# Kernel optimization log

Measured on AMD Instinct MI355X. Metric: run time of the kernel, lower is better.

Reference implementation:

```python
import jax, jax.numpy as jnp
import numpy as np
import math

N, D = 4096, 1024


def setup_inputs() -> dict:
    key = jax.random.key(0)
    ks = jax.random.split(key, 8)
    vecs = jax.random.normal(ks[0], (N, D), dtype=jnp.float32)
    mass = jax.random.uniform(ks[1], (N,), dtype=jnp.float32)            # semantic mass in [0,1)
    hops = jax.random.uniform(ks[2], (N,), dtype=jnp.float32) * 5.0      # hop distances in [0,5)
    alive = jax.random.randint(ks[3], (N,), 0, 10) > 0
    is_photon = jax.random.randint(ks[4], (N,), 0, 10) == 0
    W_res_w = jax.random.normal(ks[5], (D, D), dtype=jnp.float32) / np.sqrt(D)
    W_res_b = jnp.zeros((D,), dtype=jnp.float32)
    w_conf_i = jax.random.normal(ks[6], (D,), dtype=jnp.float32) / np.sqrt(2 * D)
    w_conf_j = jax.random.normal(ks[7], (D,), dtype=jnp.float32) / np.sqrt(2 * D)
    b_conf = jnp.zeros((), dtype=jnp.float32)
    log_c = jnp.asarray(math.log(50.0), dtype=jnp.float32)  # 'relationship' domain
    log_G = jnp.zeros((), dtype=jnp.float32)
    return dict(vecs=vecs, mass=mass, hops=hops, alive=alive, is_photon=is_photon,
                W_res_w=W_res_w, W_res_b=W_res_b, w_conf_i=w_conf_i, w_conf_j=w_conf_j,
                b_conf=b_conf, log_c=log_c, log_G=log_G)


def reference(vecs, mass, hops, alive, is_photon, W_res_w, W_res_b,
              w_conf_i, w_conf_j, b_conf, log_c, log_G):
    n = vecs.shape[0]
    c = jnp.maximum(jnp.exp(log_c), 1e-6)
    G = jnp.exp(log_G)

    # Per-row quantities (phi() reads hops/photon from entity i).
    d_light = hops / c                                                   # [N]
    lam = jnp.where(is_photon, 1.0, jnp.exp(-d_light))                   # redshift, [N]
    r2 = jnp.maximum(d_light, 0.1) ** 2                                  # r_safe^2, [N]
    causal_decay = jnp.where(d_light <= 1.0, 1.0, jnp.exp(-d_light + 1.0))  # [N]

    # Causal mask: j must be strictly in the past (j < i).
    idx = jnp.arange(n)
    past = (idx[None, :] < idx[:, None]).astype(vecs.dtype)              # [N,N]
    C = past * causal_decay[:, None]

    # Gravity: G * m_i * m_j / r_i^2
    grav = G * (mass / r2)[:, None] * mass[None, :]                      # [N,N]

    # Resonance: cosine similarity of W_res projections (torch eps=1e-8 norm clamp).
    v = vecs @ W_res_w.T + W_res_b                                       # [N,D]
    vn = v / jnp.maximum(jnp.linalg.norm(v, axis=-1, keepdims=True), 1e-8)
    R = vn @ vn.T                                                        # [N,N]
    zero_norm = jnp.linalg.norm(vecs, axis=-1) < 1e-8                    # [N]
    R = jnp.where(zero_norm[:, None] | zero_norm[None, :], 0.0, R)

    # Conflict gate: sigmoid(W_conflict @ concat(v_i, v_j) + b) = sigmoid(s_i + s_j + b).
    s_i = vecs @ w_conf_i                                                # [N]
    s_j = vecs @ w_conf_j                                                # [N]
    conflict = jax.nn.sigmoid(s_i[:, None] + s_j[None, :] + b_conf)      # [N,N]

    phi_attract = lam[:, None] * grav * C * (0.5 + 0.5 * R)
    phi_repulse = -lam[:, None] * conflict * mass[:, None] * mass[None, :]
    phi = jnp.where(conflict > 0.8, phi_repulse, phi_attract)

    # Black holes and the diagonal produce zero field.
    gate = alive[:, None] & alive[None, :]
    phi = jnp.where(gate & (idx[:, None] != idx[None, :]), phi, 0.0)
    return phi
```

## Files before the change

### kernel.cpp

```cpp
#include <hip/hip_runtime.h>
#include <hip/hip_bf16.h>
#include <math.h>

#define NROW 4096
#define DIM  1024

typedef short v8s __attribute__((ext_vector_type(8)));
typedef float v4f __attribute__((ext_vector_type(4)));

#define GLD16(src, dst) __builtin_amdgcn_global_load_lds( \
    (const __attribute__((address_space(1))) void*)(src), \
    (__attribute__((address_space(3))) void*)(dst), 16, 0, 0)

__device__ __forceinline__ ushort f2bf(float f) {
    __hip_bfloat16 h = __float2bfloat16(f);
    union { __hip_bfloat16 h; ushort u; } x; x.h = h; return x.u;
}
__device__ __forceinline__ ushort4 cvt4(float4 a) {
    ushort4 r; r.x = f2bf(a.x); r.y = f2bf(a.y); r.z = f2bf(a.z); r.w = f2bf(a.w);
    return r;
}

__global__ __launch_bounds__(256) void k_stats(
    const float* __restrict__ vecs, const float* __restrict__ mass,
    const float* __restrict__ hops, const int* __restrict__ alive,
    const int* __restrict__ is_photon, const float* __restrict__ wci,
    const float* __restrict__ wcj, const float* __restrict__ logc,
    const float* __restrict__ logG, const float* __restrict__ bconf,
    const float* __restrict__ W,
    double* __restrict__ s_i, double* __restrict__ s_j,
    float* __restrict__ rowAtt, float* __restrict__ rowRep,
    float* __restrict__ massF, int* __restrict__ flags,
    float* __restrict__ rownorm)
{
    const int t = threadIdx.x;
    const int wid = t >> 6, lane = t & 63;

    if (blockIdx.x >= NROW / 4) {
        const int row = (blockIdx.x - NROW / 4) * 4 + wid;
        const float* wr = W + (size_t)row * DIM;
        ushort4 uc[4];
        #pragma unroll
        for (int q = 0; q < 4; ++q)
            uc[q] = cvt4(*(const float4*)&wr[lane * 4 + q * 256]);
        __syncthreads();
        ushort* wb = (ushort*)W + (size_t)row * 2048 + 1024;
        #pragma unroll
        for (int q = 0; q < 4; ++q)
            *(ushort4*)&wb[lane * 4 + q * 256] = uc[q];
        return;
    }

    const int row = blockIdx.x * 4 + wid;
    const float* vr = vecs + (size_t)row * DIM;
    double di = 0.0, dj = 0.0, ss = 0.0;
    ushort4 uc[4];
    #pragma unroll
    for (int q = 0; q < 4; ++q) {
        int base = lane * 4 + q * 256;
        float4 pv = *(const float4*)&vr[base];
        float4 pi = *(const float4*)&wci[base];
        float4 pj = *(const float4*)&wcj[base];
        di += (double)pv.x * pi.x + (double)pv.y * pi.y + (double)pv.z * pi.z + (double)pv.w * pi.w;
        dj += (double)pv.x * pj.x + (double)pv.y * pj.y + (double)pv.z * pj.z + (double)pv.w * pj.w;
        ss += (double)pv.x * pv.x + (double)pv.y * pv.y + (double)pv.z * pv.z + (double)pv.w * pv.w;
        uc[q] = cvt4(pv);
    }
    __syncthreads();
    ushort* vb = (ushort*)vecs + (size_t)row * 2048 + 1024;
    #pragma unroll
    for (int q = 0; q < 4; ++q)
        *(ushort4*)&vb[lane * 4 + q * 256] = uc[q];
    #pragma unroll
    for (int off = 32; off > 0; off >>= 1) {
        di += __shfl_down(di, off);
        dj += __shfl_down(dj, off);
        ss += __shfl_down(ss, off);
    }
    if (lane == 0) {
        double c  = fmax(exp((double)logc[0]), 1e-6);
        double G  = exp((double)logG[0]);
        double dl = (double)hops[row] / c;
        double lam = (is_photon[row] != 0) ? 1.0 : exp(-dl);
        double rs  = fmax(dl, 0.1);
        double cd  = (dl <= 1.0) ? 1.0 : exp(-dl + 1.0);
        double m   = (double)mass[row];
        s_i[row] = di;
        s_j[row] = dj + (double)bconf[0];
        rowAtt[row] = (float)(lam * G * m / (rs * rs) * cd);
        rowRep[row] = (float)(-lam * m);
        massF[row]  = (float)m;
        flags[row]  = ((alive[row] != 0) ? 1 : 0) | ((sqrt(ss) < 1e-8) ? 2 : 0);
        rownorm[row] = 0.0f;
    }
}

__global__ __launch_bounds__(256) void k_proj(
    const float* __restrict__ A, const float* __restrict__ B,
    const float* __restrict__ bias, ushort* __restrict__ vout,
    float* __restrict__ rownorm)
{
    __shared__ ushort As[64 * 64], Bs[64 * 64];
    const int t = threadIdx.x;
    const int m0 = blockIdx.y * 64, n0 = blockIdx.x * 64;
    const int wid = t >> 6, lane = t & 63;
    const int wm = wid >> 1, wn = wid & 1;
    const int quad = lane >> 4, l16 = lane & 15;
    const ushort* Ab = (const ushort*)A;
    const ushort* Bb = (const ushort*)B;
    const int sr = t >> 3;
    const int sc = t & 7;
    v4f acc[2][2];
    #pragma unroll
    for (int i = 0; i < 2; i++)
        #pragma unroll
        for (int j = 0; j < 2; j++) acc[i][j] = (v4f){0.f, 0.f, 0.f, 0.f};

    for (int k0 = 0; k0 < DIM; k0 += 64) {
        #pragma unroll
        for (int p = 0; p < 2; ++p) {
            int r = p * 32 + sr;
            int ksw = ((sc ^ (r & 7)) * 8);
            GLD16(&Ab[(size_t)(m0 + r) * 2048 + 1024 + k0 + ksw], &As[p * 2048 + wid * 512]);
            GLD16(&Bb[(size_t)(n0 + r) * 2048 + 1024 + k0 + ksw], &Bs[p * 2048 + wid * 512]);
        }
        __syncthreads();
        #pragma unroll
        for (int ks = 0; ks < 2; ++ks) {
            v8s af[2], bfr[2];
            #pragma unroll
            for (int mi = 0; mi < 2; mi++) {
                int row = wm * 32 + mi * 16 + l16;
                af[mi] = *(const v8s*)&As[row * 64 + (((ks * 4 + quad) ^ (l16 & 7)) * 8)];
            }
            #pragma unroll
            for (int ni = 0; ni < 2; ni++) {
                int row = wn * 32 + ni * 16 + l16;
                bfr[ni] = *(const v8s*)&Bs[row * 64 + (((ks * 4 + quad) ^ (l16 & 7)) * 8)];
            }
            #pragma unroll
            for (int mi = 0; mi < 2; mi++)
                #pragma unroll
                for (int ni = 0; ni < 2; ni++)
                    acc[mi][ni] = __builtin_amdgcn_mfma_f32_16x16x32_bf16(af[mi], bfr[ni], acc[mi][ni], 0, 0, 0);
        }
        __syncthreads();
    }
    float bcol[2];
    #pragma unroll
    for (int ni = 0; ni < 2; ni++) bcol[ni] = bias[n0 + wn * 32 + ni * 16 + l16];
    #pragma unroll
    for (int mi = 0; mi < 2; mi++)
        #pragma unroll
        for (int r = 0; r < 4; r++) {
            int row = m0 + wm * 32 + mi * 16 + quad * 4 + r;
            float ss = 0.0f;
            #pragma unroll
            for (int ni = 0; ni < 2; ni++) {
                int col = n0 + wn * 32 + ni * 16 + l16;
                float vv = acc[mi][ni][r] + bcol[ni];
                vout[(size_t)row * DIM + col] = f2bf(vv);
                ss += vv * vv;
            }
            #pragma unroll
            for (int off = 8; off > 0; off >>= 1) ss += __shfl_down(ss, off);
            if (l16 == 0) atomicAdd(&rownorm[row], ss);
        }
}

__global__ __launch_bounds__(256) void k_phi(
    const ushort* __restrict__ vn,
    const double* __restrict__ s_i, const double* __restrict__ s_j,
    const float* __restrict__ rowAtt, const float* __restrict__ rowRep,
    const float* __restrict__ massF, const int* __restrict__ flags,
    const float* __restrict__ rownorm, float* __restrict__ out)
{
    __shared__ ushort As[128 * 64], Bs[128 * 64];
    const int t = threadIdx.x;
    const int id = blockIdx.x;
    int r = 0;
    while (id >= ((r + 1) * (r + 2)) >> 1) ++r;
    const int bi = r, bj = id - ((r * (r + 1)) >> 1);
    const int m0 = bi * 128, n0 = bj * 128;
    const int wid = t >> 6, lane = t & 63;
    const int wm = wid >> 1, wn = wid & 1;
    const int quad = lane >> 4, l16 = lane & 15;
    const double LN4 = 1.3862943611198906;

    if (id < 496) {
        int l = id, rl = 0;
        while (l >= 31 - rl) { l -= 31 - rl; ++rl; }
        const int lm0 = rl * 128, ln0 = (rl + 1 + l) * 128;
        float cmL[4]; double csjL[4]; int cfL[4]; int ccolL[4];
        #pragma unroll
        for (int ni = 0; ni < 4; ni++) {
            int col = ln0 + wn * 64 + ni * 16 + l16;
            ccolL[ni] = col; cmL[ni] = massF[col]; csjL[ni] = s_j[col]; cfL[ni] = flags[col];
        }
        #pragma unroll
        for (int mi = 0; mi < 4; mi++)
            #pragma unroll
            for (int rr = 0; rr < 4; rr++) {
                int row = lm0 + wm * 64 + mi * 16 + quad * 4 + rr;
                float  rR = rowRep[row];
                int    fi = flags[row];
                double si = s_i[row];
                size_t ob = (size_t)row * NROW;
                #pragma unroll
                for (int ni = 0; ni < 4; ni++) {
                    double x = si + csjL[ni];
                    bool   hit = (x > LN4) && ((fi & cfL[ni]) & 1);
                    float  conflict = 1.0f / (1.0f + expf(-(float)x));
                    out[ob + ccolL[ni]] = hit ? rR * conflict * cmL[ni] : 0.0f;
                }
            }
    }

    float  cm[4]; double csj[4]; int cf[4]; int ccol[4];
    #pragma unroll
    for (int ni = 0; ni < 4; ni++) {
        int col = n0 + wn * 64 + ni * 16 + l16;
        ccol[ni] = col; cm[ni] = massF[col]; csj[ni] = s_j[col]; cf[ni] = flags[col];
    }

    v4f acc[4][4];
    #pragma unroll
    for (int i = 0; i < 4; i++)
        #pragma unroll
        for (int j = 0; j < 4; j++) acc[i][j] = (v4f){0.f, 0.f, 0.f, 0.f};

    const int sr = t >> 3;
    const int sc = t & 7;
    for (int k0 = 0; k0 < DIM; k0 += 64) {
        #pragma unroll
        for (int p = 0; p < 4; ++p) {
            int rr = p * 32 + sr;
            int ksw = ((sc ^ (rr & 7)) * 8);
            GLD16(&vn[(size_t)(m0 + rr) * DIM + k0 + ksw], &As[p * 2048 + wid * 512]);
            GLD16(&vn[(size_t)(n0 + rr) * DIM + k0 + ksw], &Bs[p * 2048 + wid * 512]);
        }
        __syncthreads();
        #pragma unroll
        for (int ks = 0; ks < 2; ++ks) {
            v8s af[4], bfr[4];
            #pragma unroll
            for (int mi = 0; mi < 4; mi++) {
                int row = wm * 64 + mi * 16 + l16;
                af[mi] = *(const v8s*)&As[row * 64 + (((ks * 4 + quad) ^ (l16 & 7)) * 8)];
            }
            #pragma unroll
            for (int ni = 0; ni < 4; ni++) {
                int row = wn * 64 + ni * 16 + l16;
                bfr[ni] = *(const v8s*)&Bs[row * 64 + (((ks * 4 + quad) ^ (l16 & 7)) * 8)];
            }
            #pragma unroll
            for (int mi = 0; mi < 4; mi++)
                #pragma unroll
                for (int ni = 0; ni < 4; ni++)
                    acc[mi][ni] = __builtin_amdgcn_mfma_f32_16x16x32_bf16(af[mi], bfr[ni], acc[mi][ni], 0, 0, 0);
        }
        __syncthreads();
    }

    float cinv[4];
    #pragma unroll
    for (int ni = 0; ni < 4; ni++)
        cinv[ni] = 1.0f / fmaxf(sqrtf(rownorm[ccol[ni]]), 1e-8f);

    #pragma unroll
    for (int mi = 0; mi < 4; mi++)
        #pragma unroll
        for (int rr = 0; rr < 4; rr++) {
            int row = m0 + wm * 64 + mi * 16 + quad * 4 + rr;
            float  rA = rowAtt[row], rR = rowRep[row];
            float  riv = 1.0f / fmaxf(sqrtf(rownorm[row]), 1e-8f);
            int    fi = flags[row];
            double si = s_i[row];
            size_t ob = (size_t)row * NROW;
            #pragma unroll
            for (int ni = 0; ni < 4; ni++) {
                int col = ccol[ni];
                double x = si + csj[ni];
                float conflict = 1.0f / (1.0f + expf(-(float)x));
                bool  chigh = x > LN4;
                bool  gate  = ((fi & cf[ni]) & 1) && (row != col);
                float Rv  = ((fi | cf[ni]) & 2) ? 0.0f : acc[mi][ni][rr] * riv * cinv[ni];
                float att = (col < row) ? rA * cm[ni] * (0.5f + 0.5f * Rv) : 0.0f;
                float ph  = gate ? (chigh ? rR * conflict * cm[ni] : att) : 0.0f;
                out[ob + col] = ph;
            }
        }
}

extern "C" void kernel_launch(void* const* d_in, const int* in_sizes, int n_in,
                              void* d_out, int out_size, void* d_ws, size_t ws_size,
                              hipStream_t stream)
{
    const float* vecs      = (const float*)d_in[0];
    const float* mass      = (const float*)d_in[1];
    const float* hops      = (const float*)d_in[2];
    const int*   alive     = (const int*)d_in[3];
    const int*   is_photon = (const int*)d_in[4];
    const float* W         = (const float*)d_in[5];
    const float* Wb        = (const float*)d_in[6];
    const float* wci       = (const float*)d_in[7];
    const float* wcj       = (const float*)d_in[8];
    const float* bconf     = (const float*)d_in[9];
    const float* logc      = (const float*)d_in[10];
    const float* logG      = (const float*)d_in[11];

    char* ws = (char*)d_ws;
    double* s_i     = (double*)(ws);
    double* s_j     = (double*)(ws + 32768);
    float*  rowAtt  = (float*)(ws + 65536);
    float*  rowRep  = (float*)(ws + 81920);
    float*  massF   = (float*)(ws + 98304);
    int*    flagsA  = (int*)(ws + 114688);
    float*  rownorm = (float*)(ws + 131072);
    ushort* vn      = (ushort*)(ws + 147456);

    k_stats<<<dim3(NROW / 4 + DIM / 4), dim3(256), 0, stream>>>(
        vecs, mass, hops, alive, is_photon, wci, wcj, logc, logG, bconf, W,
        s_i, s_j, rowAtt, rowRep, massF, flagsA, rownorm);
    k_proj<<<dim3(DIM / 64, NROW / 64), dim3(256), 0, stream>>>(vecs, W, Wb, vn, rownorm);
    k_phi<<<dim3(528), dim3(256), 0, stream>>>(
        vn, s_i, s_j, rowAtt, rowRep, massF, flagsA, rownorm, (float*)d_out);
}
```

Baseline: 184.4 us.

## Shrink phi tiles to 64x64, fold mirror tile writes and precompute per-row/col factors

The phi kernel moves from 128x128 to 64x64 output tiles over the lower triangle (2080 blocks instead of 528). Each off-diagonal block now also writes the mirrored upper-triangle repulse-only tile, so a separate group of 496 blocks is no longer needed. Alive and zero-norm masks and the norm reciprocals are folded into precomputed per-row and per-column factors, and fast exp and rcp intrinsics replace the exact ones. The first K tile is prefetched before the loop and occupancy is raised with launch bounds, at the cost of less data reuse per block and more LDS barriers per unit of work.

```diff
diff --git a/kernel.cpp b/kernel.cpp
--- a/kernel.cpp
+++ b/kernel.cpp
@@ -168,126 +168,147 @@
         }
 }
 
-__global__ __launch_bounds__(256) void k_phi(
+__global__ __launch_bounds__(256, 5) void k_phi(
     const ushort* __restrict__ vn,
     const double* __restrict__ s_i, const double* __restrict__ s_j,
     const float* __restrict__ rowAtt, const float* __restrict__ rowRep,
     const float* __restrict__ massF, const int* __restrict__ flags,
     const float* __restrict__ rownorm, float* __restrict__ out)
 {
-    __shared__ ushort As[128 * 64], Bs[128 * 64];
+    __shared__ ushort As[64 * 64], Bs[64 * 64];
     const int t = threadIdx.x;
     const int id = blockIdx.x;
-    int r = 0;
-    while (id >= ((r + 1) * (r + 2)) >> 1) ++r;
+    int r = (int)((sqrtf(8.0f * (float)id + 1.0f) - 1.0f) * 0.5f);
+    while ((((r + 1) * (r + 2)) >> 1) <= id) ++r;
+    while (((r * (r + 1)) >> 1) > id) --r;
     const int bi = r, bj = id - ((r * (r + 1)) >> 1);
-    const int m0 = bi * 128, n0 = bj * 128;
+    const bool diag = (bi == bj);
+    const int m0 = bi * 64, n0 = bj * 64;
     const int wid = t >> 6, lane = t & 63;
     const int wm = wid >> 1, wn = wid & 1;
     const int quad = lane >> 4, l16 = lane & 15;
+    const int sr = t >> 3, sc = t & 7;
     const double LN4 = 1.3862943611198906;
 
-    if (id < 496) {
-        int l = id, rl = 0;
-        while (l >= 31 - rl) { l -= 31 - rl; ++rl; }
-        const int lm0 = rl * 128, ln0 = (rl + 1 + l) * 128;
-        float cmL[4]; double csjL[4]; int cfL[4]; int ccolL[4];
-        #pragma unroll
-        for (int ni = 0; ni < 4; ni++) {
-            int col = ln0 + wn * 64 + ni * 16 + l16;
-            ccolL[ni] = col; cmL[ni] = massF[col]; csjL[ni] = s_j[col]; cfL[ni] = flags[col];
-        }
-        #pragma unroll
-        for (int mi = 0; mi < 4; mi++)
+    #pragma unroll
+    for (int p = 0; p < 2; ++p) {
+        int rr = p * 32 + sr;
+        int ksw = (sc ^ (rr & 7)) * 8;
+        GLD16(&vn[(size_t)(m0 + rr) * DIM + ksw], &As[p * 2048 + wid * 512]);
+        GLD16(&vn[(size_t)(n0 + rr) * DIM + ksw], &Bs[p * 2048 + wid * 512]);
+    }
+
+    if (!diag) {
+        double csjL[2]; float cmL[2]; int colL[2];
+        #pragma unroll
+        for (int ni = 0; ni < 2; ni++) {
+            int col = m0 + wn * 32 + ni * 16 + l16;
+            colL[ni] = col;
+            csjL[ni] = s_j[col];
+            cmL[ni]  = (flags[col] & 1) ? massF[col] : 0.f;
+        }
+        #pragma unroll
+        for (int mi = 0; mi < 2; mi++)
             #pragma unroll
             for (int rr = 0; rr < 4; rr++) {
-                int row = lm0 + wm * 64 + mi * 16 + quad * 4 + rr;
-                float  rR = rowRep[row];
-                int    fi = flags[row];
+                int row = n0 + wm * 32 + mi * 16 + quad * 4 + rr;
                 double si = s_i[row];
+                float  rRm = (flags[row] & 1) ? rowRep[row] : 0.f;
                 size_t ob = (size_t)row * NROW;
                 #pragma unroll
-                for (int ni = 0; ni < 4; ni++) {
+                for (int ni = 0; ni < 2; ni++) {
                     double x = si + csjL[ni];
-                    bool   hit = (x > LN4) && ((fi & cfL[ni]) & 1);
-                    float  conflict = 1.0f / (1.0f + expf(-(float)x));
-                    out[ob + ccolL[ni]] = hit ? rR * conflict * cmL[ni] : 0.0f;
+                    float v = 0.f;
+                    if (x > LN4) {
+                        float e = __expf(-(float)x);
+                        v = rRm * cmL[ni] * __builtin_amdgcn_rcpf(1.0f + e);
+                    }
+                    out[ob + colL[ni]] = v;
                 }
             }
     }
 
-    float  cm[4]; double csj[4]; int cf[4]; int ccol[4];
-    #pragma unroll
-    for (int ni = 0; ni < 4; ni++) {
-        int col = n0 + wn * 64 + ni * 16 + l16;
-        ccol[ni] = col; cm[ni] = massF[col]; csj[ni] = s_j[col]; cf[ni] = flags[col];
-    }
-
-    v4f acc[4][4];
-    #pragma unroll
-    for (int i = 0; i < 4; i++)
-        #pragma unroll
-        for (int j = 0; j < 4; j++) acc[i][j] = (v4f){0.f, 0.f, 0.f, 0.f};
-
-    const int sr = t >> 3;
-    const int sc = t & 7;
+    double csjH[2]; float cmn[2], cc[2]; int colH[2];
+    #pragma unroll
+    for (int ni = 0; ni < 2; ni++) {
+        int col = n0 + wn * 32 + ni * 16 + l16;
+        int cf = flags[col];
+        float cma = (cf & 1) ? massF[col] : 0.f;
+        colH[ni] = col;
+        csjH[ni] = s_j[col];
+        cmn[ni]  = cma;
+        cc[ni]   = (cf & 2) ? 0.f
+                 : cma * __builtin_amdgcn_rcpf(fmaxf(sqrtf(rownorm[col]), 1e-8f));
+    }
+
+    v4f acc[2][2];
+    #pragma unroll
+    for (int i = 0; i < 2; i++)
+        #pragma unroll
+        for (int j = 0; j < 2; j++) acc[i][j] = (v4f){0.f, 0.f, 0.f, 0.f};
+
+    __syncthreads();
     for (int k0 = 0; k0 < DIM; k0 += 64) {
         #pragma unroll
-        for (int p = 0; p < 4; ++p) {
-            int rr = p * 32 + sr;
-            int ksw = ((sc ^ (rr & 7)) * 8);
-            GLD16(&vn[(size_t)(m0 + rr) * DIM + k0 + ksw], &As[p * 2048 + wid * 512]);
-            GLD16(&vn[(size_t)(n0 + rr) * DIM + k0 + ksw], &Bs[p * 2048 + wid * 512]);
-        }
-        __syncthreads();
-        #pragma unroll
         for (int ks = 0; ks < 2; ++ks) {
-            v8s af[4], bfr[4];
-            #pragma unroll
-            for (int mi = 0; mi < 4; mi++) {
-                int row = wm * 64 + mi * 16 + l16;
+            v8s af[2], bfr[2];
+            #pragma unroll
+            for (int mi = 0; mi < 2; mi++) {
+                int row = wm * 32 + mi * 16 + l16;
                 af[mi] = *(const v8s*)&As[row * 64 + (((ks * 4 + quad) ^ (l16 & 7)) * 8)];
             }
             #pragma unroll
-            for (int ni = 0; ni < 4; ni++) {
-                int row = wn * 64 + ni * 16 + l16;
+            for (int ni = 0; ni < 2; ni++) {
+                int row = wn * 32 + ni * 16 + l16;
                 bfr[ni] = *(const v8s*)&Bs[row * 64 + (((ks * 4 + quad) ^ (l16 & 7)) * 8)];
             }
             #pragma unroll
-            for (int mi = 0; mi < 4; mi++)
+            for (int mi = 0; mi < 2; mi++)
                 #pragma unroll
-                for (int ni = 0; ni < 4; ni++)
+                for (int ni = 0; ni < 2; ni++)
                     acc[mi][ni] = __builtin_amdgcn_mfma_f32_16x16x32_bf16(af[mi], bfr[ni], acc[mi][ni], 0, 0, 0);
         }
-        __syncthreads();
-    }
-
-    float cinv[4];
-    #pragma unroll
-    for (int ni = 0; ni < 4; ni++)
-        cinv[ni] = 1.0f / fmaxf(sqrtf(rownorm[ccol[ni]]), 1e-8f);
-
-    #pragma unroll
-    for (int mi = 0; mi < 4; mi++)
+        if (k0 + 64 < DIM) {
+            __syncthreads();
+            int k1 = k0 + 64;
+            #pragma unroll
+            for (int p = 0; p < 2; ++p) {
+                int rr = p * 32 + sr;
+                int ksw = (sc ^ (rr & 7)) * 8;
+                GLD16(&vn[(size_t)(m0 + rr) * DIM + k1 + ksw], &As[p * 2048 + wid * 512]);
+                GLD16(&vn[(size_t)(n0 + rr) * DIM + k1 + ksw], &Bs[p * 2048 + wid * 512]);
+            }
+            __syncthreads();
+        }
+    }
+
+    #pragma unroll
+    for (int mi = 0; mi < 2; mi++)
         #pragma unroll
         for (int rr = 0; rr < 4; rr++) {
-            int row = m0 + wm * 64 + mi * 16 + quad * 4 + rr;
-            float  rA = rowAtt[row], rR = rowRep[row];
-            float  riv = 1.0f / fmaxf(sqrtf(rownorm[row]), 1e-8f);
-            int    fi = flags[row];
+            int row = m0 + wm * 32 + mi * 16 + quad * 4 + rr;
+            int fi = flags[row];
+            float rA  = rowAtt[row];
+            float riv = __builtin_amdgcn_rcpf(fmaxf(sqrtf(rownorm[row]), 1e-8f));
+            float a1  = (fi & 1) ? 0.5f * rA : 0.f;
+            float a2  = ((fi & 3) == 1) ? 0.5f * rA * riv : 0.f;
+            float rRm = (fi & 1) ? rowRep[row] : 0.f;
             double si = s_i[row];
             size_t ob = (size_t)row * NROW;
             #pragma unroll
-            for (int ni = 0; ni < 4; ni++) {
-                int col = ccol[ni];
-                double x = si + csj[ni];
-                float conflict = 1.0f / (1.0f + expf(-(float)x));
-                bool  chigh = x > LN4;
-                bool  gate  = ((fi & cf[ni]) & 1) && (row != col);
-                float Rv  = ((fi | cf[ni]) & 2) ? 0.0f : acc[mi][ni][rr] * riv * cinv[ni];
-                float att = (col < row) ? rA * cm[ni] * (0.5f + 0.5f * Rv) : 0.0f;
-                float ph  = gate ? (chigh ? rR * conflict * cm[ni] : att) : 0.0f;
-                out[ob + col] = ph;
+            for (int ni = 0; ni < 2; ni++) {
+                double x = si + csjH[ni];
+                float  acv = acc[mi][ni][rr];
+                float  att = fmaf(a2 * cc[ni], acv, a1 * cmn[ni]);
+                float  e   = __expf(-(float)x);
+                float  rep = rRm * cmn[ni] * __builtin_amdgcn_rcpf(1.0f + e);
+                float  v   = (x > LN4) ? rep : att;
+                if (diag) {
+                    int col = colH[ni];
+                    if (col > row) v = (x > LN4) ? rep : 0.f;
+                    if (col == row) v = 0.f;
+                }
+                out[ob + colH[ni]] = v;
             }
         }
 }
@@ -323,6 +344,6 @@
         vecs, mass, hops, alive, is_photon, wci, wcj, logc, logG, bconf, W,
         s_i, s_j, rowAtt, rowRep, massF, flagsA, rownorm);
     k_proj<<<dim3(DIM / 64, NROW / 64), dim3(256), 0, stream>>>(vecs, W, Wb, vn, rownorm);
-    k_phi<<<dim3(528), dim3(256), 0, stream>>>(
+    k_phi<<<dim3(2080), dim3(256), 0, stream>>>(
         vn, s_i, s_j, rowAtt, rowRep, massF, flagsA, rownorm, (float*)d_out);
 }
```

Measured after the change: 167.6 us. -9.1%, faster.
